# Kernel optimization log

Hardware: AMD Instinct MI355X
Metric: run time of the kernel (lower is better)

The kernel has to match this reference:

```python
import jax, jax.numpy as jnp
import numpy as np
from jax import lax

T, IN, H, OUT = 4096, 32, 512, 32


def _lstm_layer(x_seq, W_ih, W_hh, b_ih, b_hh):
    # x_seq: [T, D_in]; PyTorch gate order: i, f, g, o
    Hd = W_hh.shape[1]
    b = b_ih + b_hh

    def step(carry, x):
        h, c = carry
        gates = x @ W_ih.T + h @ W_hh.T + b  # [4H]
        i, f, g, o = jnp.split(gates, 4)
        i = jax.nn.sigmoid(i)
        f = jax.nn.sigmoid(f)
        g = jnp.tanh(g)
        o = jax.nn.sigmoid(o)
        c2 = f * c + i * g
        h2 = o * jnp.tanh(c2)
        return (h2, c2), h2

    init = (jnp.zeros((Hd,), x_seq.dtype), jnp.zeros((Hd,), x_seq.dtype))
    _, hs = lax.scan(step, init, x_seq)
    return hs  # [T, Hd]


def setup_inputs() -> dict:
    key = jax.random.key(0)
    ks = jax.random.split(key, 16)
    s = 0.05
    return {
        "seq": jax.random.normal(ks[0], (T, IN), jnp.float32),
        "W_ih1": jax.random.normal(ks[1], (4 * H, IN), jnp.float32) * s,
        "W_hh1": jax.random.normal(ks[2], (4 * H, H), jnp.float32) * s,
        "b_ih1": jax.random.normal(ks[3], (4 * H,), jnp.float32) * s,
        "b_hh1": jax.random.normal(ks[4], (4 * H,), jnp.float32) * s,
        "W_ih2": jax.random.normal(ks[5], (4 * H, H), jnp.float32) * s,
        "W_hh2": jax.random.normal(ks[6], (4 * H, H), jnp.float32) * s,
        "b_ih2": jax.random.normal(ks[7], (4 * H,), jnp.float32) * s,
        "b_hh2": jax.random.normal(ks[8], (4 * H,), jnp.float32) * s,
        "W_ih3": jax.random.normal(ks[9], (4 * H, H), jnp.float32) * s,
        "W_hh3": jax.random.normal(ks[10], (4 * H, H), jnp.float32) * s,
        "b_ih3": jax.random.normal(ks[11], (4 * H,), jnp.float32) * s,
        "b_hh3": jax.random.normal(ks[12], (4 * H,), jnp.float32) * s,
        "W_out": jax.random.normal(ks[13], (OUT, H), jnp.float32) * s,
        "b_out": jax.random.normal(ks[14], (OUT,), jnp.float32) * s,
    }


def reference(seq, W_ih1, W_hh1, b_ih1, b_hh1, W_ih2, W_hh2, b_ih2, b_hh2,
              W_ih3, W_hh3, b_ih3, b_hh3, W_out, b_out):
    h1 = _lstm_layer(seq, W_ih1, W_hh1, b_ih1, b_hh1)  # [T, H]
    h2 = _lstm_layer(h1, W_ih2, W_hh2, b_ih2, b_hh2)   # [T, H]
    h3 = _lstm_layer(h2, W_ih3, W_hh3, b_ih3, b_hh3)   # [T, H]
    return h3 @ W_out.T + b_out  # [T, OUT]
```

## Files before the change

kernel.cpp:

```cpp
#include <hip/hip_runtime.h>


#define T_SEQ 4096
#define HDIM  512
#define NWG_L 32
#define NTH   1024

typedef unsigned long long u64;

__device__ __forceinline__ u64 cohLoad(const u64* p) {
    return __hip_atomic_load(p, __ATOMIC_RELAXED, __HIP_MEMORY_SCOPE_AGENT);
}
__device__ __forceinline__ void cohStore(u64* p, u64 v) {
    __hip_atomic_store(p, v, __ATOMIC_RELAXED, __HIP_MEMORY_SCOPE_AGENT);
}
__device__ __forceinline__ float fsigmoid(float x) {
    return __builtin_amdgcn_rcpf(1.f + __expf(-x));
}
__device__ __forceinline__ float ftanh(float x) {
    float e = __expf(2.f * fabsf(x));
    float t = 1.f - 2.f * __builtin_amdgcn_rcpf(e + 1.f);
    return copysignf(t, x);
}

template <int BM, int BN, int BK>
__global__ __launch_bounds__(256)
void gemm_abt(const float* __restrict__ A, const float* __restrict__ B,
              const float* __restrict__ bias1,
              float* __restrict__ C, int M, int N, int K) {
    constexpr int NTX = BN / 4;
    constexpr int NTY = 256 / NTX;
    constexpr int TM  = BM / NTY;
    __shared__ float As[BM][BK + 1];
    __shared__ float Bs[BN][BK + 1];

    const int tid = threadIdx.x;
    const int tx = tid % NTX;
    const int ty = tid / NTX;
    const int m0 = blockIdx.y * BM;
    const int n0 = blockIdx.x * BN;

    float acc[TM][4];
    #pragma unroll
    for (int i = 0; i < TM; ++i)
        #pragma unroll
        for (int j = 0; j < 4; ++j) acc[i][j] = 0.f;

    for (int k0 = 0; k0 < K; k0 += BK) {
        constexpr int AV = BM * BK / 4;
        #pragma unroll
        for (int i = tid; i < AV; i += 256) {
            int r = i / (BK / 4), c4 = i % (BK / 4);
            float4 v = *(const float4*)(A + (size_t)(m0 + r) * K + k0 + c4 * 4);
            As[r][c4 * 4 + 0] = v.x; As[r][c4 * 4 + 1] = v.y;
            As[r][c4 * 4 + 2] = v.z; As[r][c4 * 4 + 3] = v.w;
        }
        constexpr int BV = BN * BK / 4;
        #pragma unroll
        for (int i = tid; i < BV; i += 256) {
            int r = i / (BK / 4), c4 = i % (BK / 4);
            float4 v = *(const float4*)(B + (size_t)(n0 + r) * K + k0 + c4 * 4);
            Bs[r][c4 * 4 + 0] = v.x; Bs[r][c4 * 4 + 1] = v.y;
            Bs[r][c4 * 4 + 2] = v.z; Bs[r][c4 * 4 + 3] = v.w;
        }
        __syncthreads();
        #pragma unroll
        for (int kk = 0; kk < BK; ++kk) {
            float a[TM], b[4];
            #pragma unroll
            for (int i = 0; i < TM; ++i) a[i] = As[ty * TM + i][kk];
            #pragma unroll
            for (int j = 0; j < 4; ++j) b[j] = Bs[tx * 4 + j][kk];
            #pragma unroll
            for (int i = 0; i < TM; ++i)
                #pragma unroll
                for (int j = 0; j < 4; ++j) acc[i][j] += a[i] * b[j];
        }
        __syncthreads();
    }

    #pragma unroll
    for (int j = 0; j < 4; ++j) {
        float bv = bias1 ? bias1[n0 + tx * 4 + j] : 0.f;
        #pragma unroll
        for (int i = 0; i < TM; ++i) acc[i][j] += bv;
    }
    #pragma unroll
    for (int i = 0; i < TM; ++i) {
        int m = m0 + ty * TM + i;
        float4 v = make_float4(acc[i][0], acc[i][1], acc[i][2], acc[i][3]);
        *(float4*)(C + (size_t)m * N + n0 + tx * 4) = v;
    }
}

__global__ void unpack_h(const u64* __restrict__ hp, float* __restrict__ out,
                         int n) {
    int i = blockIdx.x * blockDim.x + threadIdx.x;
    if (i < n) out[i] = __uint_as_float((unsigned)hp[i]);
}

__global__ __launch_bounds__(NTH, 4)
void lstm_fused(const float* __restrict__ seq,
                const float* __restrict__ Wih1, const float* __restrict__ Whh1,
                const float* __restrict__ bih1, const float* __restrict__ bhh1,
                const float* __restrict__ Wih2, const float* __restrict__ Whh2,
                const float* __restrict__ bih2, const float* __restrict__ bhh2,
                const float* __restrict__ Wih3, const float* __restrict__ Whh3,
                const float* __restrict__ bih3, const float* __restrict__ bhh3,
                u64* __restrict__ hp) {
    __shared__ __align__(16) float h_in[2][1024 + 32];
    __shared__ float part[16 * 64];

    const int blk   = blockIdx.x;
    const int layer = blk >> 5;
    const int g     = blk & 31;
    const int tid   = threadIdx.x;
    const int wv    = tid >> 6;
    const int lane  = tid & 63;
    const int gate  = lane >> 4;
    const int cl    = lane & 15;
    const int grow  = gate * HDIM + g * 16 + cl;

    const float* Wih = layer == 0 ? Wih1 : (layer == 1 ? Wih2 : Wih3);
    const float* Whh = layer == 0 ? Whh1 : (layer == 1 ? Whh2 : Whh3);
    const float* bih = layer == 0 ? bih1 : (layer == 1 ? bih2 : bih3);
    const float* bhh = layer == 0 ? bhh1 : (layer == 1 ? bhh2 : bhh3);

    float w[64];
    #pragma unroll
    for (int m = 0; m < 64; ++m) w[m] = 0.f;
    if (layer == 0) {
        const float* wp = Whh + (size_t)grow * HDIM + wv * 32;
        #pragma unroll
        for (int i = 0; i < 8; ++i) {
            float4 v = ((const float4*)wp)[i];
            w[4*i+0]=v.x; w[4*i+1]=v.y; w[4*i+2]=v.z; w[4*i+3]=v.w;
        }
        float2 xw = *(const float2*)(Wih + (size_t)grow * 32 + 2 * wv);
        w[32] = xw.x; w[33] = xw.y;
    } else {
        const float* wp = (wv < 8)
            ? Wih + (size_t)grow * HDIM + wv * 64
            : Whh + (size_t)grow * HDIM + (wv - 8) * 64;
        #pragma unroll
        for (int i = 0; i < 16; ++i) {
            float4 v = ((const float4*)wp)[i];
            w[4*i+0]=v.x; w[4*i+1]=v.y; w[4*i+2]=v.z; w[4*i+3]=v.w;
        }
    }
    #pragma unroll
    for (int m = 0; m < 64; ++m) asm volatile("" : "+v"(w[m]));

    const float brow = bih[grow] + bhh[grow];

    u64*       hpOwn  = hp + (size_t)layer * T_SEQ * HDIM;
    const u64* hpPrev = hp + (size_t)(layer > 0 ? layer - 1 : 0) * T_SEQ * HDIM;

    float c = 0.f;

    for (unsigned t = 0; t < T_SEQ; ++t) {
        const int pb = t & 1;
        if (layer == 0) {
            if (tid < HDIM) {
                float hv = 0.f;
                if (t > 0) {
                    const u64* ph = hpOwn + (size_t)(t - 1) * HDIM + tid;
                    u64 v;
                    do { v = cohLoad(ph); } while ((unsigned)(v >> 32) != t);
                    hv = __uint_as_float((unsigned)v);
                }
                h_in[pb][tid] = hv;
            } else if (tid < HDIM + 32) {
                h_in[pb][tid] = seq[(size_t)t * 32 + (tid - HDIM)];
            }
        } else {
            if (tid < HDIM) {
                const u64* px = hpPrev + (size_t)t * HDIM + tid;
                u64 v;
                do { v = cohLoad(px); } while ((unsigned)(v >> 32) != t + 1u);
                h_in[pb][tid] = __uint_as_float((unsigned)v);
            } else {
                float hv = 0.f;
                if (t > 0) {
                    const u64* ph = hpOwn + (size_t)(t - 1) * HDIM + (tid - HDIM);
                    u64 v;
                    do { v = cohLoad(ph); } while ((unsigned)(v >> 32) != t);
                    hv = __uint_as_float((unsigned)v);
                }
                h_in[pb][tid] = hv;
            }
        }
        __syncthreads();

        float p = 0.f;
        if (layer == 0) {
            const float4* base = (const float4*)(h_in[pb]) + wv * 8;
            #pragma unroll
            for (int i = 0; i < 8; ++i) {
                float4 hv = base[i];
                p += w[4*i+0]*hv.x + w[4*i+1]*hv.y
                   + w[4*i+2]*hv.z + w[4*i+3]*hv.w;
            }
            float2 xv = ((const float2*)(h_in[pb] + HDIM))[wv];
            p += w[32]*xv.x + w[33]*xv.y;
        } else {
            const float4* base = (const float4*)(h_in[pb]) + wv * 16;
            #pragma unroll
            for (int i = 0; i < 16; ++i) {
                float4 hv = base[i];
                p += w[4*i+0]*hv.x + w[4*i+1]*hv.y
                   + w[4*i+2]*hv.z + w[4*i+3]*hv.w;
            }
        }
        part[wv * 64 + lane] = p;
        __syncthreads();

        if (wv == 0) {
            float tot = brow;
            #pragma unroll
            for (int wvv = 0; wvv < 16; ++wvv) tot += part[wvv * 64 + lane];
            float ai = __shfl(tot, cl +  0, 64);
            float af = __shfl(tot, cl + 16, 64);
            float ag = __shfl(tot, cl + 32, 64);
            float ao = __shfl(tot, cl + 48, 64);
            if (lane < 16) {
                float iv = fsigmoid(ai);
                float fv = fsigmoid(af);
                float gv = ftanh(ag);
                float ov = fsigmoid(ao);
                c = fv * c + iv * gv;
                float h = ov * ftanh(c);
                u64 pkt = (u64)__float_as_uint(h) | ((u64)(t + 1u) << 32);
                cohStore(hpOwn + (size_t)t * HDIM + g * 16 + lane, pkt);
            }
        }
    }
}

extern "C" void kernel_launch(void* const* d_in, const int* in_sizes, int n_in,
                              void* d_out, int out_size, void* d_ws, size_t ws_size,
                              hipStream_t stream) {
    const float* seq   = (const float*)d_in[0];
    const float* W_ih1 = (const float*)d_in[1];
    const float* W_hh1 = (const float*)d_in[2];
    const float* b_ih1 = (const float*)d_in[3];
    const float* b_hh1 = (const float*)d_in[4];
    const float* W_ih2 = (const float*)d_in[5];
    const float* W_hh2 = (const float*)d_in[6];
    const float* b_ih2 = (const float*)d_in[7];
    const float* b_hh2 = (const float*)d_in[8];
    const float* W_ih3 = (const float*)d_in[9];
    const float* W_hh3 = (const float*)d_in[10];
    const float* b_ih3 = (const float*)d_in[11];
    const float* b_hh3 = (const float*)d_in[12];
    const float* W_out = (const float*)d_in[13];
    const float* b_out = (const float*)d_in[14];
    float* out = (float*)d_out;

    u64*   hp   = (u64*)d_ws;
    float* hs2f = (float*)d_ws;
    const u64* hp2 = hp + (size_t)2 * T_SEQ * HDIM;

    hipMemsetAsync(hp, 0, (size_t)3 * T_SEQ * HDIM * sizeof(u64), stream);

    lstm_fused<<<3 * NWG_L, NTH, 0, stream>>>(
        seq, W_ih1, W_hh1, b_ih1, b_hh1, W_ih2, W_hh2, b_ih2, b_hh2,
        W_ih3, W_hh3, b_ih3, b_hh3, hp);

    const int n = T_SEQ * HDIM;
    unpack_h<<<(n + 255) / 256, 256, 0, stream>>>(hp2, hs2f, n);

    gemm_abt<64, 32, 32><<<dim3(1, T_SEQ / 64), 256, 0, stream>>>(
        hs2f, W_out, b_out, out, T_SEQ, 32, HDIM);
}
```

Measured before the change: 7.618 ms.

## Reassign each lane to a k-slice over four gate rows with shuffle reduction

Restructures the per-block matvec so each lane owns a 16-column, 8- or 16-wide k-slice for all four gates, reusing each h_in vector load across four gate rows. Partial sums are reduced across the wave with xor shuffles, and only 16 lanes per wave write a float4 to shared memory. This reduces LDS reads of the hidden state per step, at the cost of extra shuffles, more register pressure (wx array), and strided final reads from the partial buffer.

```diff
diff --git a/kernel.cpp b/kernel.cpp
--- a/kernel.cpp
+++ b/kernel.cpp
@@ -109,7 +109,7 @@
                 const float* __restrict__ bih3, const float* __restrict__ bhh3,
                 u64* __restrict__ hp) {
     __shared__ __align__(16) float h_in[2][1024 + 32];
-    __shared__ float part[16 * 64];
+    __shared__ __align__(16) float part[16 * 16 * 4];
 
     const int blk   = blockIdx.x;
     const int layer = blk >> 5;
@@ -117,41 +117,64 @@
     const int tid   = threadIdx.x;
     const int wv    = tid >> 6;
     const int lane  = tid & 63;
+    const int sub   = lane >> 4;
+    const int cl    = lane & 15;
+    const int chunk = wv * 4 + sub;
     const int gate  = lane >> 4;
-    const int cl    = lane & 15;
-    const int grow  = gate * HDIM + g * 16 + cl;
+    const int col0  = g * 16 + cl;
 
     const float* Wih = layer == 0 ? Wih1 : (layer == 1 ? Wih2 : Wih3);
     const float* Whh = layer == 0 ? Whh1 : (layer == 1 ? Whh2 : Whh3);
     const float* bih = layer == 0 ? bih1 : (layer == 1 ? bih2 : bih3);
     const float* bhh = layer == 0 ? bhh1 : (layer == 1 ? bhh2 : bhh3);
 
-    float w[64];
-    #pragma unroll
-    for (int m = 0; m < 64; ++m) w[m] = 0.f;
+    float wh[64];
+    float wx[16];
+    #pragma unroll
+    for (int m = 0; m < 64; ++m) wh[m] = 0.f;
+    #pragma unroll
+    for (int m = 0; m < 16; ++m) wx[m] = 0.f;
+
     if (layer == 0) {
-        const float* wp = Whh + (size_t)grow * HDIM + wv * 32;
-        #pragma unroll
-        for (int i = 0; i < 8; ++i) {
-            float4 v = ((const float4*)wp)[i];
-            w[4*i+0]=v.x; w[4*i+1]=v.y; w[4*i+2]=v.z; w[4*i+3]=v.w;
-        }
-        float2 xw = *(const float2*)(Wih + (size_t)grow * 32 + 2 * wv);
-        w[32] = xw.x; w[33] = xw.y;
+        const int k0 = chunk * 8;
+        #pragma unroll
+        for (int r = 0; r < 4; ++r) {
+            const float* wp = Whh + (size_t)(r * HDIM + col0) * HDIM + k0;
+            #pragma unroll
+            for (int k4 = 0; k4 < 2; ++k4) {
+                float4 v = ((const float4*)wp)[k4];
+                wh[r*8 + 4*k4 + 0] = v.x; wh[r*8 + 4*k4 + 1] = v.y;
+                wh[r*8 + 4*k4 + 2] = v.z; wh[r*8 + 4*k4 + 3] = v.w;
+            }
+        }
+        if (chunk < 8) {
+            #pragma unroll
+            for (int r = 0; r < 4; ++r) {
+                float4 v = *(const float4*)(Wih + (size_t)(r * HDIM + col0) * 32
+                                            + chunk * 4);
+                wx[r*4+0]=v.x; wx[r*4+1]=v.y; wx[r*4+2]=v.z; wx[r*4+3]=v.w;
+            }
+        }
     } else {
-        const float* wp = (wv < 8)
-            ? Wih + (size_t)grow * HDIM + wv * 64
-            : Whh + (size_t)grow * HDIM + (wv - 8) * 64;
-        #pragma unroll
-        for (int i = 0; i < 16; ++i) {
-            float4 v = ((const float4*)wp)[i];
-            w[4*i+0]=v.x; w[4*i+1]=v.y; w[4*i+2]=v.z; w[4*i+3]=v.w;
-        }
-    }
-    #pragma unroll
-    for (int m = 0; m < 64; ++m) asm volatile("" : "+v"(w[m]));
-
-    const float brow = bih[grow] + bhh[grow];
+        const float* Wsrc = (chunk < 32) ? Wih : Whh;
+        const int k0 = (chunk < 32 ? chunk : chunk - 32) * 16;
+        #pragma unroll
+        for (int r = 0; r < 4; ++r) {
+            const float* wp = Wsrc + (size_t)(r * HDIM + col0) * HDIM + k0;
+            #pragma unroll
+            for (int k4 = 0; k4 < 4; ++k4) {
+                float4 v = ((const float4*)wp)[k4];
+                wh[r*16 + 4*k4 + 0] = v.x; wh[r*16 + 4*k4 + 1] = v.y;
+                wh[r*16 + 4*k4 + 2] = v.z; wh[r*16 + 4*k4 + 3] = v.w;
+            }
+        }
+    }
+    #pragma unroll
+    for (int m = 0; m < 64; ++m) asm volatile("" : "+v"(wh[m]));
+    #pragma unroll
+    for (int m = 0; m < 16; ++m) asm volatile("" : "+v"(wx[m]));
+
+    const float brow = bih[gate * HDIM + col0] + bhh[gate * HDIM + col0];
 
     u64*       hpOwn  = hp + (size_t)layer * T_SEQ * HDIM;
     const u64* hpPrev = hp + (size_t)(layer > 0 ? layer - 1 : 0) * T_SEQ * HDIM;
@@ -192,33 +215,59 @@
         }
         __syncthreads();
 
-        float p = 0.f;
+        float p0 = 0.f, p1 = 0.f, p2 = 0.f, p3 = 0.f;
         if (layer == 0) {
-            const float4* base = (const float4*)(h_in[pb]) + wv * 8;
-            #pragma unroll
-            for (int i = 0; i < 8; ++i) {
-                float4 hv = base[i];
-                p += w[4*i+0]*hv.x + w[4*i+1]*hv.y
-                   + w[4*i+2]*hv.z + w[4*i+3]*hv.w;
-            }
-            float2 xv = ((const float2*)(h_in[pb] + HDIM))[wv];
-            p += w[32]*xv.x + w[33]*xv.y;
+            const float4* hb = (const float4*)(h_in[pb]) + chunk * 2;
+            #pragma unroll
+            for (int k4 = 0; k4 < 2; ++k4) {
+                float4 hv = hb[k4];
+                p0 += wh[0*8+4*k4+0]*hv.x + wh[0*8+4*k4+1]*hv.y
+                    + wh[0*8+4*k4+2]*hv.z + wh[0*8+4*k4+3]*hv.w;
+                p1 += wh[1*8+4*k4+0]*hv.x + wh[1*8+4*k4+1]*hv.y
+                    + wh[1*8+4*k4+2]*hv.z + wh[1*8+4*k4+3]*hv.w;
+                p2 += wh[2*8+4*k4+0]*hv.x + wh[2*8+4*k4+1]*hv.y
+                    + wh[2*8+4*k4+2]*hv.z + wh[2*8+4*k4+3]*hv.w;
+                p3 += wh[3*8+4*k4+0]*hv.x + wh[3*8+4*k4+1]*hv.y
+                    + wh[3*8+4*k4+2]*hv.z + wh[3*8+4*k4+3]*hv.w;
+            }
+            if (chunk < 8) {
+                float4 xv = ((const float4*)(h_in[pb] + HDIM))[chunk];
+                p0 += wx[0]*xv.x + wx[1]*xv.y + wx[2]*xv.z + wx[3]*xv.w;
+                p1 += wx[4]*xv.x + wx[5]*xv.y + wx[6]*xv.z + wx[7]*xv.w;
+                p2 += wx[8]*xv.x + wx[9]*xv.y + wx[10]*xv.z + wx[11]*xv.w;
+                p3 += wx[12]*xv.x + wx[13]*xv.y + wx[14]*xv.z + wx[15]*xv.w;
+            }
         } else {
-            const float4* base = (const float4*)(h_in[pb]) + wv * 16;
-            #pragma unroll
-            for (int i = 0; i < 16; ++i) {
-                float4 hv = base[i];
-                p += w[4*i+0]*hv.x + w[4*i+1]*hv.y
-                   + w[4*i+2]*hv.z + w[4*i+3]*hv.w;
-            }
-        }
-        part[wv * 64 + lane] = p;
+            const float4* hb = (const float4*)(h_in[pb]) + chunk * 4;
+            #pragma unroll
+            for (int k4 = 0; k4 < 4; ++k4) {
+                float4 hv = hb[k4];
+                p0 += wh[0*16+4*k4+0]*hv.x + wh[0*16+4*k4+1]*hv.y
+                    + wh[0*16+4*k4+2]*hv.z + wh[0*16+4*k4+3]*hv.w;
+                p1 += wh[1*16+4*k4+0]*hv.x + wh[1*16+4*k4+1]*hv.y
+                    + wh[1*16+4*k4+2]*hv.z + wh[1*16+4*k4+3]*hv.w;
+                p2 += wh[2*16+4*k4+0]*hv.x + wh[2*16+4*k4+1]*hv.y
+                    + wh[2*16+4*k4+2]*hv.z + wh[2*16+4*k4+3]*hv.w;
+                p3 += wh[3*16+4*k4+0]*hv.x + wh[3*16+4*k4+1]*hv.y
+                    + wh[3*16+4*k4+2]*hv.z + wh[3*16+4*k4+3]*hv.w;
+            }
+        }
+
+        p0 += __shfl_xor(p0, 16, 64); p1 += __shfl_xor(p1, 16, 64);
+        p2 += __shfl_xor(p2, 16, 64); p3 += __shfl_xor(p3, 16, 64);
+        p0 += __shfl_xor(p0, 32, 64); p1 += __shfl_xor(p1, 32, 64);
+        p2 += __shfl_xor(p2, 32, 64); p3 += __shfl_xor(p3, 32, 64);
+        if (lane < 16) {
+            float4 st = make_float4(p0, p1, p2, p3);
+            ((float4*)part)[wv * 16 + lane] = st;
+        }
         __syncthreads();
 
         if (wv == 0) {
             float tot = brow;
             #pragma unroll
-            for (int wvv = 0; wvv < 16; ++wvv) tot += part[wvv * 64 + lane];
+            for (int wvv = 0; wvv < 16; ++wvv)
+                tot += part[wvv * 64 + cl * 4 + gate];
             float ai = __shfl(tot, cl +  0, 64);
             float af = __shfl(tot, cl + 16, 64);
             float ag = __shfl(tot, cl + 32, 64);
```

Result: slower. 13.67 ms (+79.5%).

## Remap lanes to compute two gate rows per thread over smaller k-chunks

Applied to the files above, without the earlier changes.

Each lane now owns two gate rows (i/f paired with g/o) across a k-chunk half the previous width, with the two half-wavefronts covering adjacent chunks. This halves the shared-memory h reads per output row, since one float4 load of h feeds two rows' FMAs. Partial sums are first combined across half-waves with a shuffle, then written to shared memory as float2. The cost is an extra cross-lane shuffle, a more complex indexing scheme for the final reduction, and possible LDS bank conflicts from the interleaved layout.

```diff
diff --git a/kernel.cpp b/kernel.cpp
--- a/kernel.cpp
+++ b/kernel.cpp
@@ -109,7 +109,7 @@
                 const float* __restrict__ bih3, const float* __restrict__ bhh3,
                 u64* __restrict__ hp) {
     __shared__ __align__(16) float h_in[2][1024 + 32];
-    __shared__ float part[16 * 64];
+    __shared__ __align__(16) float part[16 * 64];
 
     const int blk   = blockIdx.x;
     const int layer = blk >> 5;
@@ -117,41 +117,54 @@
     const int tid   = threadIdx.x;
     const int wv    = tid >> 6;
     const int lane  = tid & 63;
-    const int gate  = lane >> 4;
-    const int cl    = lane & 15;
-    const int grow  = gate * HDIM + g * 16 + cl;
+    const int sg    = lane >> 5;
+    const int cl    = lane & 31;
+    const int chunk = wv * 2 + sg;
 
     const float* Wih = layer == 0 ? Wih1 : (layer == 1 ? Wih2 : Wih3);
     const float* Whh = layer == 0 ? Whh1 : (layer == 1 ? Whh2 : Whh3);
     const float* bih = layer == 0 ? bih1 : (layer == 1 ? bih2 : bih3);
     const float* bhh = layer == 0 ? bhh1 : (layer == 1 ? bhh2 : bhh3);
 
+    const int grow0 = (cl >> 4) * HDIM + g * 16 + (cl & 15);
+    const int grow1 = (2 + (cl >> 4)) * HDIM + g * 16 + (cl & 15);
+
     float w[64];
     #pragma unroll
     for (int m = 0; m < 64; ++m) w[m] = 0.f;
     if (layer == 0) {
-        const float* wp = Whh + (size_t)grow * HDIM + wv * 32;
-        #pragma unroll
-        for (int i = 0; i < 8; ++i) {
-            float4 v = ((const float4*)wp)[i];
-            w[4*i+0]=v.x; w[4*i+1]=v.y; w[4*i+2]=v.z; w[4*i+3]=v.w;
-        }
-        float2 xw = *(const float2*)(Wih + (size_t)grow * 32 + 2 * wv);
-        w[32] = xw.x; w[33] = xw.y;
+        const int k0 = chunk * 16;
+        const float* wp0 = Whh + (size_t)grow0 * HDIM + k0;
+        const float* wp1 = Whh + (size_t)grow1 * HDIM + k0;
+        #pragma unroll
+        for (int k4 = 0; k4 < 4; ++k4) {
+            float4 v0 = ((const float4*)wp0)[k4];
+            w[4*k4+0]=v0.x; w[4*k4+1]=v0.y; w[4*k4+2]=v0.z; w[4*k4+3]=v0.w;
+            float4 v1 = ((const float4*)wp1)[k4];
+            w[16+4*k4+0]=v1.x; w[16+4*k4+1]=v1.y;
+            w[16+4*k4+2]=v1.z; w[16+4*k4+3]=v1.w;
+        }
+        w[32] = Wih[(size_t)grow0 * 32 + chunk];
+        w[33] = Wih[(size_t)grow1 * 32 + chunk];
     } else {
-        const float* wp = (wv < 8)
-            ? Wih + (size_t)grow * HDIM + wv * 64
-            : Whh + (size_t)grow * HDIM + (wv - 8) * 64;
-        #pragma unroll
-        for (int i = 0; i < 16; ++i) {
-            float4 v = ((const float4*)wp)[i];
-            w[4*i+0]=v.x; w[4*i+1]=v.y; w[4*i+2]=v.z; w[4*i+3]=v.w;
+        const float* Wsrc = (chunk < 16) ? Wih : Whh;
+        const int k0 = (chunk & 15) * 32;
+        const float* wp0 = Wsrc + (size_t)grow0 * HDIM + k0;
+        const float* wp1 = Wsrc + (size_t)grow1 * HDIM + k0;
+        #pragma unroll
+        for (int k4 = 0; k4 < 8; ++k4) {
+            float4 v0 = ((const float4*)wp0)[k4];
+            w[4*k4+0]=v0.x; w[4*k4+1]=v0.y; w[4*k4+2]=v0.z; w[4*k4+3]=v0.w;
+            float4 v1 = ((const float4*)wp1)[k4];
+            w[32+4*k4+0]=v1.x; w[32+4*k4+1]=v1.y;
+            w[32+4*k4+2]=v1.z; w[32+4*k4+3]=v1.w;
         }
     }
     #pragma unroll
     for (int m = 0; m < 64; ++m) asm volatile("" : "+v"(w[m]));
 
-    const float brow = bih[grow] + bhh[grow];
+    const float brow = bih[(lane >> 4) * HDIM + g * 16 + (lane & 15)]
+                     + bhh[(lane >> 4) * HDIM + g * 16 + (lane & 15)];
 
     u64*       hpOwn  = hp + (size_t)layer * T_SEQ * HDIM;
     const u64* hpPrev = hp + (size_t)(layer > 0 ? layer - 1 : 0) * T_SEQ * HDIM;
@@ -192,37 +205,48 @@
         }
         __syncthreads();
 
-        float p = 0.f;
+        float p0 = 0.f, p1 = 0.f;
         if (layer == 0) {
-            const float4* base = (const float4*)(h_in[pb]) + wv * 8;
-            #pragma unroll
-            for (int i = 0; i < 8; ++i) {
-                float4 hv = base[i];
-                p += w[4*i+0]*hv.x + w[4*i+1]*hv.y
-                   + w[4*i+2]*hv.z + w[4*i+3]*hv.w;
-            }
-            float2 xv = ((const float2*)(h_in[pb] + HDIM))[wv];
-            p += w[32]*xv.x + w[33]*xv.y;
+            const float4* hb = (const float4*)(h_in[pb]) + chunk * 4;
+            #pragma unroll
+            for (int k4 = 0; k4 < 4; ++k4) {
+                float4 hv = hb[k4];
+                p0 += w[4*k4+0]*hv.x + w[4*k4+1]*hv.y
+                    + w[4*k4+2]*hv.z + w[4*k4+3]*hv.w;
+                p1 += w[16+4*k4+0]*hv.x + w[16+4*k4+1]*hv.y
+                    + w[16+4*k4+2]*hv.z + w[16+4*k4+3]*hv.w;
+            }
+            float xval = h_in[pb][HDIM + chunk];
+            p0 += w[32] * xval;
+            p1 += w[33] * xval;
         } else {
-            const float4* base = (const float4*)(h_in[pb]) + wv * 16;
-            #pragma unroll
-            for (int i = 0; i < 16; ++i) {
-                float4 hv = base[i];
-                p += w[4*i+0]*hv.x + w[4*i+1]*hv.y
-                   + w[4*i+2]*hv.z + w[4*i+3]*hv.w;
-            }
-        }
-        part[wv * 64 + lane] = p;
+            const float4* hb = (const float4*)(h_in[pb]) + chunk * 8;
+            #pragma unroll
+            for (int k4 = 0; k4 < 8; ++k4) {
+                float4 hv = hb[k4];
+                p0 += w[4*k4+0]*hv.x + w[4*k4+1]*hv.y
+                    + w[4*k4+2]*hv.z + w[4*k4+3]*hv.w;
+                p1 += w[32+4*k4+0]*hv.x + w[32+4*k4+1]*hv.y
+                    + w[32+4*k4+2]*hv.z + w[32+4*k4+3]*hv.w;
+            }
+        }
+
+        p0 += __shfl_xor(p0, 32, 64);
+        p1 += __shfl_xor(p1, 32, 64);
+        if (lane < 32)
+            ((float2*)part)[wv * 32 + lane] = make_float2(p0, p1);
         __syncthreads();
 
         if (wv == 0) {
             float tot = brow;
             #pragma unroll
-            for (int wvv = 0; wvv < 16; ++wvv) tot += part[wvv * 64 + lane];
-            float ai = __shfl(tot, cl +  0, 64);
-            float af = __shfl(tot, cl + 16, 64);
-            float ag = __shfl(tot, cl + 32, 64);
-            float ao = __shfl(tot, cl + 48, 64);
+            for (int wvv = 0; wvv < 16; ++wvv)
+                tot += part[wvv * 64 + (lane & 31) * 2 + (lane >> 5)];
+            const int c16 = lane & 15;
+            float ai = __shfl(tot, c16 +  0, 64);
+            float af = __shfl(tot, c16 + 16, 64);
+            float ag = __shfl(tot, c16 + 32, 64);
+            float ao = __shfl(tot, c16 + 48, 64);
             if (lane < 16) {
                 float iv = fsigmoid(ai);
                 float fv = fsigmoid(af);
```

After: 13.85 ms. +81.9%, slower.

## Broadcast hidden state via readlane instead of LDS staging and barrier

Applied to the files above, without the earlier changes.

Each wave now loads its own slice of the previous hidden state directly from the coherent buffer and broadcasts values across lanes with readlane, removing the shared h_in staging array and one __syncthreads per timestep. The partial-sum buffer is double-buffered by timestep parity so the remaining single barrier suffices. Layer 0 input projection is moved entirely to wave 15, which gives that wave extra work. The intent is to shorten the serial per-step latency of the recurrence.

```diff
diff --git a/kernel.cpp b/kernel.cpp
--- a/kernel.cpp
+++ b/kernel.cpp
@@ -21,6 +21,9 @@
     float e = __expf(2.f * fabsf(x));
     float t = 1.f - 2.f * __builtin_amdgcn_rcpf(e + 1.f);
     return copysignf(t, x);
+}
+__device__ __forceinline__ float bcast(float v, int k) {
+    return __uint_as_float(__builtin_amdgcn_readlane(__float_as_uint(v), k));
 }
 
 template <int BM, int BN, int BK>
@@ -108,8 +111,7 @@
                 const float* __restrict__ Wih3, const float* __restrict__ Whh3,
                 const float* __restrict__ bih3, const float* __restrict__ bhh3,
                 u64* __restrict__ hp) {
-    __shared__ __align__(16) float h_in[2][1024 + 32];
-    __shared__ float part[16 * 64];
+    __shared__ float part[2][NTH];
 
     const int blk   = blockIdx.x;
     const int layer = blk >> 5;
@@ -117,9 +119,7 @@
     const int tid   = threadIdx.x;
     const int wv    = tid >> 6;
     const int lane  = tid & 63;
-    const int gate  = lane >> 4;
-    const int cl    = lane & 15;
-    const int grow  = gate * HDIM + g * 16 + cl;
+    const int grow  = (lane >> 4) * HDIM + g * 16 + (lane & 15);
 
     const float* Wih = layer == 0 ? Wih1 : (layer == 1 ? Wih2 : Wih3);
     const float* Whh = layer == 0 ? Whh1 : (layer == 1 ? Whh2 : Whh3);
@@ -136,8 +136,15 @@
             float4 v = ((const float4*)wp)[i];
             w[4*i+0]=v.x; w[4*i+1]=v.y; w[4*i+2]=v.z; w[4*i+3]=v.w;
         }
-        float2 xw = *(const float2*)(Wih + (size_t)grow * 32 + 2 * wv);
-        w[32] = xw.x; w[33] = xw.y;
+        if (wv == 15) {
+            const float* xp = Wih + (size_t)grow * 32;
+            #pragma unroll
+            for (int i = 0; i < 8; ++i) {
+                float4 v = ((const float4*)xp)[i];
+                w[32+4*i+0]=v.x; w[32+4*i+1]=v.y;
+                w[32+4*i+2]=v.z; w[32+4*i+3]=v.w;
+            }
+        }
     } else {
         const float* wp = (wv < 8)
             ? Wih + (size_t)grow * HDIM + wv * 64
@@ -160,69 +167,66 @@
 
     for (unsigned t = 0; t < T_SEQ; ++t) {
         const int pb = t & 1;
+
+        float hval = 0.f;
+        float xval = 0.f;
         if (layer == 0) {
-            if (tid < HDIM) {
-                float hv = 0.f;
-                if (t > 0) {
-                    const u64* ph = hpOwn + (size_t)(t - 1) * HDIM + tid;
-                    u64 v;
-                    do { v = cohLoad(ph); } while ((unsigned)(v >> 32) != t);
-                    hv = __uint_as_float((unsigned)v);
-                }
-                h_in[pb][tid] = hv;
-            } else if (tid < HDIM + 32) {
-                h_in[pb][tid] = seq[(size_t)t * 32 + (tid - HDIM)];
-            }
+            if (lane < 32 && t > 0) {
+                const u64* ph = hpOwn + (size_t)(t - 1) * HDIM + wv * 32 + lane;
+                u64 v;
+                do { v = cohLoad(ph); } while ((unsigned)(v >> 32) != t);
+                hval = __uint_as_float((unsigned)v);
+            }
+            if (wv == 15 && lane < 32)
+                xval = seq[(size_t)t * 32 + lane];
         } else {
-            if (tid < HDIM) {
-                const u64* px = hpPrev + (size_t)t * HDIM + tid;
+            if (wv < 8) {
+                const u64* px = hpPrev + (size_t)t * HDIM + wv * 64 + lane;
                 u64 v;
                 do { v = cohLoad(px); } while ((unsigned)(v >> 32) != t + 1u);
-                h_in[pb][tid] = __uint_as_float((unsigned)v);
-            } else {
-                float hv = 0.f;
-                if (t > 0) {
-                    const u64* ph = hpOwn + (size_t)(t - 1) * HDIM + (tid - HDIM);
-                    u64 v;
-                    do { v = cohLoad(ph); } while ((unsigned)(v >> 32) != t);
-                    hv = __uint_as_float((unsigned)v);
+                hval = __uint_as_float((unsigned)v);
+            } else if (t > 0) {
+                const u64* ph = hpOwn + (size_t)(t - 1) * HDIM
+                              + (wv - 8) * 64 + lane;
+                u64 v;
+                do { v = cohLoad(ph); } while ((unsigned)(v >> 32) != t);
+                hval = __uint_as_float((unsigned)v);
+            }
+        }
+
+        float pe = 0.f, po = 0.f;
+        if (layer == 0) {
+            #pragma unroll
+            for (int k = 0; k < 32; k += 2) {
+                pe = fmaf(bcast(hval, k),     w[k],     pe);
+                po = fmaf(bcast(hval, k + 1), w[k + 1], po);
+            }
+            if (wv == 15) {
+                #pragma unroll
+                for (int k = 0; k < 32; k += 2) {
+                    pe = fmaf(bcast(xval, k),     w[32 + k],     pe);
+                    po = fmaf(bcast(xval, k + 1), w[32 + k + 1], po);
                 }
-                h_in[pb][tid] = hv;
-            }
-        }
-        __syncthreads();
-
-        float p = 0.f;
-        if (layer == 0) {
-            const float4* base = (const float4*)(h_in[pb]) + wv * 8;
-            #pragma unroll
-            for (int i = 0; i < 8; ++i) {
-                float4 hv = base[i];
-                p += w[4*i+0]*hv.x + w[4*i+1]*hv.y
-                   + w[4*i+2]*hv.z + w[4*i+3]*hv.w;
-            }
-            float2 xv = ((const float2*)(h_in[pb] + HDIM))[wv];
-            p += w[32]*xv.x + w[33]*xv.y;
+            }
         } else {
-            const float4* base = (const float4*)(h_in[pb]) + wv * 16;
-            #pragma unroll
-            for (int i = 0; i < 16; ++i) {
-                float4 hv = base[i];
-                p += w[4*i+0]*hv.x + w[4*i+1]*hv.y
-                   + w[4*i+2]*hv.z + w[4*i+3]*hv.w;
-            }
-        }
-        part[wv * 64 + lane] = p;
+            #pragma unroll
+            for (int k = 0; k < 64; k += 2) {
+                pe = fmaf(bcast(hval, k),     w[k],     pe);
+                po = fmaf(bcast(hval, k + 1), w[k + 1], po);
+            }
+        }
+        part[pb][wv * 64 + lane] = pe + po;
         __syncthreads();
 
         if (wv == 0) {
             float tot = brow;
             #pragma unroll
-            for (int wvv = 0; wvv < 16; ++wvv) tot += part[wvv * 64 + lane];
-            float ai = __shfl(tot, cl +  0, 64);
-            float af = __shfl(tot, cl + 16, 64);
-            float ag = __shfl(tot, cl + 32, 64);
-            float ao = __shfl(tot, cl + 48, 64);
+            for (int wvv = 0; wvv < 16; ++wvv) tot += part[pb][wvv * 64 + lane];
+            const int c16 = lane & 15;
+            float ai = __shfl(tot, c16 +  0, 64);
+            float af = __shfl(tot, c16 + 16, 64);
+            float ag = __shfl(tot, c16 + 32, 64);
+            float ao = __shfl(tot, c16 + 48, 64);
             if (lane < 16) {
                 float iv = fsigmoid(ai);
                 float fv = fsigmoid(af);
```

After: 6.308 ms, median of 2. 1.21x faster.
